# Kernel optimization log

Hardware: AMD Instinct MI355X
Metric: run time of the kernel (lower is better)

Reference implementation:

```python
import math
import jax, jax.numpy as jnp
import numpy as np

BATCH = 64
N_SAMPLES = 131072
SAMPLE_RATE = 48000
CUTOFF = 1000.0
RESONANCE = 0.7


def setup_inputs() -> dict:
    key = jax.random.key(0)
    audio = jax.random.normal(key, (BATCH, N_SAMPLES), dtype=jnp.float32)
    g = jnp.asarray(math.tan(math.pi / SAMPLE_RATE * CUTOFF), dtype=jnp.float32)
    twoR = jnp.asarray(1.0 / RESONANCE, dtype=jnp.float32)
    mix = jnp.array([0.0, 1.0, 0.0], dtype=jnp.float32)  # lowpass: mix of (bp, lp, hp)
    return {"audio": audio, "g": g, "twoR": twoR, "mix": mix}


def reference(audio, g, twoR, mix):
    # audio: [batch, n_samples]; g, twoR: scalars; mix: [3]
    x = audio.T  # time-first: [n_samples, batch]
    one = jnp.ones_like(g)
    T = 1.0 / (1.0 + g * (g + twoR))
    # H = T * [[1, -g], [g, twoR*g + 1]]  (constant 2x2 transition matrix)
    H = T * jnp.stack([jnp.stack([one, -g]), jnp.stack([g, twoR * g + one])])
    gHB = g * T * jnp.stack([one, g])  # [2] input gain vector

    def step(state, x_t):
        # state: [batch, 2]; x_t: [batch]
        y = gHB[None, :] * x_t[:, None] + state @ H.T  # [batch, 2]
        return 2.0 * y - state, y

    init = jnp.zeros((x.shape[1], 2), dtype=audio.dtype)
    _, Y = jax.lax.scan(step, init, x)  # Y: [n_samples, batch, 2]

    y_bp, y_lp = Y[..., 0], Y[..., 1]
    y_hp = x - twoR * y_bp - y_lp
    y_mixed = twoR * mix[0] * y_bp + mix[1] * y_lp + mix[2] * y_hp
    return y_mixed.T  # [batch, n_samples]
```

## Files before the change

### kernel.cpp

```cpp
#include <hip/hip_runtime.h>


#define BATCH 64
#define NS    131072
#define CLEN  64
#define NCH   (NS / CLEN)
#define BPR   (NCH / 64)
#define NCOL  66
#define CST   66
#define NF4   (NCOL * CLEN / 4)
#define LD_IT ((NF4 + 63) / 64)

typedef float vfloat4 __attribute__((ext_vector_type(4)));

__global__ __launch_bounds__(64) void svf_lds(
        const float* __restrict__ audio,
        const float* __restrict__ gp,
        const float* __restrict__ twoRp,
        const float* __restrict__ mixp,
        float* __restrict__ out) {
    __shared__ float lds[NCOL * CST];

    const int lane   = threadIdx.x;
    const int b      = blockIdx.x / BPR;
    const int chunk0 = (blockIdx.x % BPR) * 64;

    const float* X = audio + (size_t)b * NS;
    float*       O = out   + (size_t)b * NS;

    const float g = gp[0], twoR = twoRp[0];
    const float T   = 1.0f / (1.0f + g * (g + twoR));
    const float h00 = T, h01 = -T * g, h10 = T * g, h11 = T * (twoR * g + 1.0f);
    const float a00 = 2.f * h00 - 1.f, a01 = 2.f * h01;
    const float a10 = 2.f * h10,       a11 = 2.f * h11 - 1.f;
    const float b0 = 2.f * g * T, b1 = 2.f * g * T * g;
    const float gb0 = g * T, gb1 = g * T * g;
    const float m0 = mixp[0], m1 = mixp[1], m2 = mixp[2];
    const float cbp = twoR * (m0 - m2), clp = m1 - m2;
    const float p  = m2 + cbp * gb0 + clp * gb1;
    const float q0 = cbp * h00 + clp * h10;
    const float q1 = cbp * h01 + clp * h11;

    const int base_f = (chunk0 - 2) * CLEN;

    vfloat4 pf[LD_IT];
#pragma unroll
    for (int i = 0; i < LD_IT; ++i) {
        const int j4 = i * 64 + lane;
        const int f  = base_f + (j4 >> 4) * CLEN + (j4 & 15) * 4;
        pf[i] = (j4 < NF4 && f >= 0)
                    ? *reinterpret_cast<const vfloat4*>(X + f)
                    : (vfloat4)(0.f);
    }
#pragma unroll
    for (int i = 0; i < LD_IT; ++i) {
        const int j4 = i * 64 + lane;
        if (j4 < NF4) {
            const int col = j4 >> 4, t4 = j4 & 15;
            float2* lp = reinterpret_cast<float2*>(&lds[col * CST + t4 * 4]);
            lp[0] = make_float2(pf[i].x, pf[i].y);
            lp[1] = make_float2(pf[i].z, pf[i].w);
        }
    }
    __syncthreads();

    float s0 = 0.f, s1 = 0.f;
    const int cbase = lane * CST;
#pragma unroll
    for (int t = 0; t < CLEN; ++t) {
        const float x  = lds[cbase + t];
        const float n0 = fmaf(a00, s0, fmaf(a01, s1, b0 * x));
        const float n1 = fmaf(a10, s0, fmaf(a11, s1, b1 * x));
        s0 = n0; s1 = n1;
    }
#pragma unroll
    for (int t = 0; t < CLEN; ++t) {
        const float x  = lds[cbase + CST + t];
        const float n0 = fmaf(a00, s0, fmaf(a01, s1, b0 * x));
        const float n1 = fmaf(a10, s0, fmaf(a11, s1, b1 * x));
        s0 = n0; s1 = n1;
    }
    __syncthreads();

    const int ebase = cbase + 2 * CST;
#pragma unroll
    for (int t = 0; t < CLEN; ++t) {
        const float x  = lds[ebase + t];
        const float o  = fmaf(p, x, fmaf(q0, s0, q1 * s1));
        const float n0 = fmaf(a00, s0, fmaf(a01, s1, b0 * x));
        const float n1 = fmaf(a10, s0, fmaf(a11, s1, b1 * x));
        s0 = n0; s1 = n1;
        lds[ebase + t] = o;
    }
    __syncthreads();

#pragma unroll
    for (int i = 0; i < 16; ++i) {
        const int j4  = i * 64 + lane;
        const int c   = j4 >> 4, t4 = j4 & 15;
        const float2* lp =
            reinterpret_cast<const float2*>(&lds[(c + 2) * CST + t4 * 4]);
        const float2 lo = lp[0], hi = lp[1];
        vfloat4 o4;
        o4.x = lo.x; o4.y = lo.y; o4.z = hi.x; o4.w = hi.y;
        const int fo = (chunk0 + c) * CLEN + t4 * 4;
        __builtin_nontemporal_store(o4, reinterpret_cast<vfloat4*>(O + fo));
    }
}

extern "C" void kernel_launch(void* const* d_in, const int* in_sizes, int n_in,
                              void* d_out, int out_size, void* d_ws, size_t ws_size,
                              hipStream_t stream) {
    const float* audio = (const float*)d_in[0];
    const float* gp    = (const float*)d_in[1];
    const float* twoRp = (const float*)d_in[2];
    const float* mixp  = (const float*)d_in[3];
    float* out = (float*)d_out;

    const int blocks = BATCH * BPR;
    svf_lds<<<blocks, 64, 0, stream>>>(audio, gp, twoRp, mixp, out);
}
```

Measured before the change: 88.13 us.

## Halve chunk length, use three-chunk halo, and vectorize LDS accesses with float4

Shrinks each lane's chunk from 64 to 32 samples, which doubles the block count and halves the serial recurrence length per thread. The warm-up halo grows from 2 to 3 chunks, so warm-up length drops from 128 to 96 samples. The LDS row stride changes to 36 floats so rows stay 16-byte aligned, and every LDS read and write becomes a float4 instead of scalars or float2 pairs. The risk is more LDS bank conflicts with the new stride, plus a larger share of redundant halo work relative to the output samples produced.

```diff
diff --git a/kernel.cpp b/kernel.cpp
--- a/kernel.cpp
+++ b/kernel.cpp
@@ -3,15 +3,24 @@
 
 #define BATCH 64
 #define NS    131072
-#define CLEN  64
-#define NCH   (NS / CLEN)
-#define BPR   (NCH / 64)
-#define NCOL  66
-#define CST   66
+#define CLEN  32
+#define NCHB  64
+#define BPR   ((NS / CLEN) / NCHB)
+#define HALO  3
+#define NCOL  (NCHB + HALO)
+#define CST   36
 #define NF4   (NCOL * CLEN / 4)
 #define LD_IT ((NF4 + 63) / 64)
 
 typedef float vfloat4 __attribute__((ext_vector_type(4)));
+
+#define SVF_STEP(xv)                                            \
+    do {                                                        \
+        const float x_ = (xv);                                  \
+        const float n0_ = fmaf(a00, s0, fmaf(a01, s1, b0 * x_));\
+        const float n1_ = fmaf(a10, s0, fmaf(a11, s1, b1 * x_));\
+        s0 = n0_; s1 = n1_;                                     \
+    } while (0)
 
 __global__ __launch_bounds__(64) void svf_lds(
         const float* __restrict__ audio,
@@ -19,11 +28,11 @@
         const float* __restrict__ twoRp,
         const float* __restrict__ mixp,
         float* __restrict__ out) {
-    __shared__ float lds[NCOL * CST];
+    __shared__ __align__(16) float lds[NCOL * CST];
 
     const int lane   = threadIdx.x;
     const int b      = blockIdx.x / BPR;
-    const int chunk0 = (blockIdx.x % BPR) * 64;
+    const int chunk0 = (blockIdx.x % BPR) * NCHB;
 
     const float* X = audio + (size_t)b * NS;
     float*       O = out   + (size_t)b * NS;
@@ -41,13 +50,13 @@
     const float q0 = cbp * h00 + clp * h10;
     const float q1 = cbp * h01 + clp * h11;
 
-    const int base_f = (chunk0 - 2) * CLEN;
+    const int base_f = (chunk0 - HALO) * CLEN;
 
     vfloat4 pf[LD_IT];
 #pragma unroll
     for (int i = 0; i < LD_IT; ++i) {
         const int j4 = i * 64 + lane;
-        const int f  = base_f + (j4 >> 4) * CLEN + (j4 & 15) * 4;
+        const int f  = base_f + (j4 >> 3) * CLEN + (j4 & 7) * 4;
         pf[i] = (j4 < NF4 && f >= 0)
                     ? *reinterpret_cast<const vfloat4*>(X + f)
                     : (vfloat4)(0.f);
@@ -56,53 +65,45 @@
     for (int i = 0; i < LD_IT; ++i) {
         const int j4 = i * 64 + lane;
         if (j4 < NF4) {
-            const int col = j4 >> 4, t4 = j4 & 15;
-            float2* lp = reinterpret_cast<float2*>(&lds[col * CST + t4 * 4]);
-            lp[0] = make_float2(pf[i].x, pf[i].y);
-            lp[1] = make_float2(pf[i].z, pf[i].w);
+            const int col = j4 >> 3, t4 = j4 & 7;
+            *reinterpret_cast<vfloat4*>(&lds[col * CST + t4 * 4]) = pf[i];
         }
     }
     __syncthreads();
 
     float s0 = 0.f, s1 = 0.f;
-    const int cbase = lane * CST;
 #pragma unroll
-    for (int t = 0; t < CLEN; ++t) {
-        const float x  = lds[cbase + t];
-        const float n0 = fmaf(a00, s0, fmaf(a01, s1, b0 * x));
-        const float n1 = fmaf(a10, s0, fmaf(a11, s1, b1 * x));
-        s0 = n0; s1 = n1;
-    }
+    for (int c = 0; c < HALO; ++c) {
+        const int cb = (lane + c) * CST;
 #pragma unroll
-    for (int t = 0; t < CLEN; ++t) {
-        const float x  = lds[cbase + CST + t];
-        const float n0 = fmaf(a00, s0, fmaf(a01, s1, b0 * x));
-        const float n1 = fmaf(a10, s0, fmaf(a11, s1, b1 * x));
-        s0 = n0; s1 = n1;
+        for (int r = 0; r < CLEN / 4; ++r) {
+            const vfloat4 x4 =
+                *reinterpret_cast<const vfloat4*>(&lds[cb + r * 4]);
+            SVF_STEP(x4.x); SVF_STEP(x4.y); SVF_STEP(x4.z); SVF_STEP(x4.w);
+        }
     }
     __syncthreads();
 
-    const int ebase = cbase + 2 * CST;
+    const int eb = (lane + HALO) * CST;
 #pragma unroll
-    for (int t = 0; t < CLEN; ++t) {
-        const float x  = lds[ebase + t];
-        const float o  = fmaf(p, x, fmaf(q0, s0, q1 * s1));
-        const float n0 = fmaf(a00, s0, fmaf(a01, s1, b0 * x));
-        const float n1 = fmaf(a10, s0, fmaf(a11, s1, b1 * x));
-        s0 = n0; s1 = n1;
-        lds[ebase + t] = o;
+    for (int r = 0; r < CLEN / 4; ++r) {
+        vfloat4* lp = reinterpret_cast<vfloat4*>(&lds[eb + r * 4]);
+        const vfloat4 x4 = *lp;
+        vfloat4 o4;
+        o4.x = fmaf(p, x4.x, fmaf(q0, s0, q1 * s1)); SVF_STEP(x4.x);
+        o4.y = fmaf(p, x4.y, fmaf(q0, s0, q1 * s1)); SVF_STEP(x4.y);
+        o4.z = fmaf(p, x4.z, fmaf(q0, s0, q1 * s1)); SVF_STEP(x4.z);
+        o4.w = fmaf(p, x4.w, fmaf(q0, s0, q1 * s1)); SVF_STEP(x4.w);
+        *lp = o4;
     }
     __syncthreads();
 
 #pragma unroll
-    for (int i = 0; i < 16; ++i) {
-        const int j4  = i * 64 + lane;
-        const int c   = j4 >> 4, t4 = j4 & 15;
-        const float2* lp =
-            reinterpret_cast<const float2*>(&lds[(c + 2) * CST + t4 * 4]);
-        const float2 lo = lp[0], hi = lp[1];
-        vfloat4 o4;
-        o4.x = lo.x; o4.y = lo.y; o4.z = hi.x; o4.w = hi.y;
+    for (int i = 0; i < NCHB * CLEN / 4 / 64; ++i) {
+        const int j4 = i * 64 + lane;
+        const int c  = j4 >> 3, t4 = j4 & 7;
+        const vfloat4 o4 =
+            *reinterpret_cast<const vfloat4*>(&lds[(c + HALO) * CST + t4 * 4]);
         const int fo = (chunk0 + c) * CLEN + t4 * 4;
         __builtin_nontemporal_store(o4, reinterpret_cast<vfloat4*>(O + fo));
     }
```

Result: no change. 86.70 us (-1.6%).
